# Optimization experiments

Measured on AMD Instinct MI355X. Metric: run time of the kernel, lower is better.

The kernel has to match this reference:

```python
import math
import jax, jax.numpy as jnp
import numpy as np

NEG_INF = -1e9

def setup_inputs() -> dict:
    key = jax.random.key(0)
    k1, k2, k3, k4, k5 = jax.random.split(key, 5)
    B, H, Q, K, D = 4, 16, 1024, 1024, 64
    return {
        "query": jax.random.normal(k1, (B, H, Q, D), dtype=jnp.float32),
        "key": jax.random.normal(k2, (B, H, K, D), dtype=jnp.float32),
        "value": jax.random.normal(k3, (B, H, K, D), dtype=jnp.float32),
        "bigr_k": jax.random.normal(k4, (Q, K, D), dtype=jnp.float32),
        "bigr_v": jax.random.normal(k5, (Q, K, D), dtype=jnp.float32),
    }

def reference(query, key, value, bigr_k, bigr_v):
    # scores: content term + relative-position key term
    scores = jnp.einsum('bhqd,bhkd->bhqk', query, key)
    scores = scores + jnp.einsum('bhqd,qkd->bhqk', query, bigr_k)
    scores = scores / math.sqrt(query.shape[-1])
    # one_direction=True -> causal (lower-triangular) mask
    Qn, Kn = scores.shape[-2], scores.shape[-1]
    causal = jnp.tril(jnp.ones((Qn, Kn), dtype=bool))
    scores = jnp.where(causal, scores, NEG_INF)
    p_attn = jax.nn.softmax(scores, axis=-1)
    output = jnp.einsum('bhqk,bhkd->bhqd', p_attn, value)
    output = output + jnp.einsum('bhqv,qvd->bhqd', p_attn, bigr_v)
    return (output, p_attn)
```

## Files before the change

kernel.cpp:

```cpp
#include <hip/hip_runtime.h>
#include <hip/hip_bf16.h>


#define BH 64
#define SQ 1024
#define SK 1024
#define DH 64
#define SCALE 0.125f

typedef __attribute__((ext_vector_type(4))) float f32x4;
typedef __attribute__((ext_vector_type(8))) unsigned short ushort8;
typedef __attribute__((ext_vector_type(8))) __bf16 bf16x8;

static __device__ inline unsigned short f2bf(float x) {
    unsigned u = __float_as_uint(x);
    unsigned r = u + 0x7FFFu + ((u >> 16) & 1u);
    return (unsigned short)(r >> 16);
}
static __device__ inline float bf2f(unsigned short s) {
    return __uint_as_float(((unsigned)s) << 16);
}

struct Frag2 { bf16x8 h, l; };

static __device__ inline Frag2 load_split(const float* __restrict__ p, float scale) {
    float4 x0 = *reinterpret_cast<const float4*>(p);
    float4 x1 = *reinterpret_cast<const float4*>(p + 4);
    float v[8] = {x0.x, x0.y, x0.z, x0.w, x1.x, x1.y, x1.z, x1.w};
    ushort8 uh, ul;
#pragma unroll
    for (int j = 0; j < 8; ++j) {
        float s = v[j] * scale;
        unsigned short h = f2bf(s);
        float r = s - bf2f(h);
        uh[j] = h;
        ul[j] = f2bf(r);
    }
    Frag2 f;
    f.h = __builtin_bit_cast(bf16x8, uh);
    f.l = __builtin_bit_cast(bf16x8, ul);
    return f;
}

static __device__ inline bf16x8 pack_bf8(float4 x0, float4 x1) {
    float v[8] = {x0.x, x0.y, x0.z, x0.w, x1.x, x1.y, x1.z, x1.w};
    ushort8 u;
#pragma unroll
    for (int j = 0; j < 8; ++j) u[j] = f2bf(v[j]);
    return __builtin_bit_cast(bf16x8, u);
}

static __device__ inline bf16x8 load_bf8(const float* __restrict__ p) {
    float4 x0 = *reinterpret_cast<const float4*>(p);
    float4 x1 = *reinterpret_cast<const float4*>(p + 4);
    return pack_bf8(x0, x1);
}

static __device__ inline bf16x8 load_bf8_strided(const float* __restrict__ p, int stride) {
    ushort8 u;
#pragma unroll
    for (int j = 0; j < 8; ++j) u[j] = f2bf(p[(size_t)j * stride]);
    return __builtin_bit_cast(bf16x8, u);
}

#define MFMA(a, b, c) __builtin_amdgcn_mfma_f32_16x16x32_bf16((a), (b), (c), 0, 0, 0)

#define GLLD(g, s)                                                              \
    __builtin_amdgcn_global_load_lds(                                           \
        (const __attribute__((address_space(1))) void*)(g),                     \
        (__attribute__((address_space(3))) void*)(s), 16, 0, 0)

#define STAGE64(src0, b)                                                        \
    do {                                                                        \
        _Pragma("unroll")                                                       \
        for (int j_ = 0; j_ < 4; ++j_) {                                        \
            const int idx_ = w * 256 + j_ * 64 + l;                             \
            const int row_ = idx_ >> 4;                                         \
            const int g_ = (idx_ & 15) ^ (row_ & 7);                            \
            GLLD((src0) + (size_t)row_ * DH + g_ * 4,                           \
                 &buf[b][w * 256 + j_ * 64]);                                   \
        }                                                                       \
    } while (0)

#define WAITVN(n)                                                               \
    do {                                                                        \
        asm volatile("s_waitcnt vmcnt(" #n ")" ::: "memory");                   \
        __builtin_amdgcn_sched_barrier(0);                                      \
    } while (0)

__global__ __launch_bounds__(256, 4) void k_scores(const float* __restrict__ qp,
                                                   const float* __restrict__ kp,
                                                   float* __restrict__ P) {
    __shared__ float4 buf[2][1024];
    const int bid = blockIdx.x;
    const int qt = bid >> 6;
    const int bh = bid & 63;
    const int tid = threadIdx.x;
    const int w = tid >> 6, l = tid & 63;
    const int lm = l & 15, lg = l >> 4;
    const int q0 = qt * 64;

    Frag2 qh0[4], qh1[4];
#pragma unroll
    for (int nt = 0; nt < 4; ++nt) {
        const float* qrow = qp + ((size_t)bh * SQ + q0 + nt * 16 + lm) * DH + lg * 8;
        qh0[nt] = load_split(qrow, SCALE);
        qh1[nt] = load_split(qrow + 32, SCALE);
    }
    const float* kb = kp + (size_t)bh * SK * DH;
    const int nt_ = qt + 1;

    STAGE64(kb, 0);
#pragma unroll 1
    for (int t = 0; t < nt_; ++t) {
        if (t + 1 < nt_) {
            STAGE64(kb + (size_t)(t + 1) * 64 * DH, (t + 1) & 1);
            WAITVN(4);
        } else {
            WAITVN(0);
        }
        const float4* L = buf[t & 1];
        const int R = w * 16 + lm;
        const int sw = R & 7;
        float4 f0 = L[R * 16 + ((2 * lg) ^ sw)];
        float4 f1 = L[R * 16 + ((2 * lg + 1) ^ sw)];
        float4 f2 = L[R * 16 + ((8 + 2 * lg) ^ sw)];
        float4 f3 = L[R * 16 + ((9 + 2 * lg) ^ sw)];
        bf16x8 alo = pack_bf8(f0, f1);
        bf16x8 ahi = pack_bf8(f2, f3);
        const int kq = t * 64 + w * 16 + lg * 4;
        const bool diag = (t == qt);
#pragma unroll
        for (int nt = 0; nt < 4; ++nt) {
            f32x4 acc = {0.f, 0.f, 0.f, 0.f};
            acc = MFMA(alo, qh0[nt].h, acc);
            acc = MFMA(alo, qh0[nt].l, acc);
            acc = MFMA(ahi, qh1[nt].h, acc);
            acc = MFMA(ahi, qh1[nt].l, acc);
            const int qe = q0 + nt * 16 + lm;
            float ov[4];
#pragma unroll
            for (int r = 0; r < 4; ++r)
                ov[r] = (!diag || (kq + r <= qe)) ? acc[r] : 0.f;
            float4 o;
            o.x = ov[0]; o.y = ov[1]; o.z = ov[2]; o.w = ov[3];
            *reinterpret_cast<float4*>(&P[((size_t)bh * SQ + qe) * SK + kq]) = o;
        }
    }
    const float4 z = {0.f, 0.f, 0.f, 0.f};
#pragma unroll 1
    for (int t = nt_; t < 16; ++t) {
        const int kq = t * 64 + w * 16 + lg * 4;
#pragma unroll
        for (int nt = 0; nt < 4; ++nt) {
            const int qe = q0 + nt * 16 + lm;
            *reinterpret_cast<float4*>(&P[((size_t)bh * SQ + qe) * SK + kq]) = z;
        }
    }
}

__global__ __launch_bounds__(256) void k_rel_pv(const float* __restrict__ query,
                                                const float* __restrict__ bigr_k,
                                                const float* __restrict__ bigr_v,
                                                float* __restrict__ P,
                                                float* __restrict__ out,
                                                float* __restrict__ rs) {
    __shared__ float4 buf[2][1024];
    __shared__ float red[4][64];
    __shared__ float rsum[64];
    int q;
    {
        const int bid = blockIdx.x, c = bid & 255;
        switch (bid >> 8) {
            case 0:  q = 1023 - c; break;
            case 1:  q = c;        break;
            case 2:  q = 767 - c;  break;
            default: q = 256 + c;  break;
        }
    }
    const int KE = q + 1;
    const int nt_ = (KE + 63) >> 6;
    const int tid = threadIdx.x;
    const int w = tid >> 6, l = tid & 63;
    const int lm = l & 15, lg = l >> 4;

    Frag2 qh0[4], qh1[4];
    float* prow[4];
#pragma unroll
    for (int nt = 0; nt < 4; ++nt) {
        const int bh = nt * 16 + lm;
        const float* qrow = query + ((size_t)bh * SQ + q) * DH + lg * 8;
        qh0[nt] = load_split(qrow, SCALE);
        qh1[nt] = load_split(qrow + 32, SCALE);
        prow[nt] = P + ((size_t)bh * SQ + q) * SK;
    }
    const float* bk = bigr_k + (size_t)q * SK * DH;
    const float* bv = bigr_v + (size_t)q * SK * DH;
    float lsum[4] = {0.f, 0.f, 0.f, 0.f};
    f32x4 pr[4][4];
#pragma unroll
    for (int a = 0; a < 4; ++a)
#pragma unroll
        for (int b = 0; b < 4; ++b) pr[a][b] = (f32x4){0.f, 0.f, 0.f, 0.f};

    STAGE64(bk, 0);
#pragma unroll 1
    for (int t = 0; t < nt_; ++t) {
        const int kq = t * 64 + w * 16 + lg * 4;
        float4 pc[4];
#pragma unroll
        for (int nt = 0; nt < 4; ++nt)
            pc[nt] = *reinterpret_cast<const float4*>(prow[nt] + kq);
        bf16x8 bvf[4];
        {
            const int kbw = t * 64 + w * 16 + 4 * lg;
#pragma unroll
            for (int ntd = 0; ntd < 4; ++ntd) {
                ushort8 u;
#pragma unroll
                for (int j = 0; j < 4; ++j)
                    u[j] = f2bf(bv[(size_t)(kbw + j) * DH + ntd * 16 + lm]);
                u[4] = 0; u[5] = 0; u[6] = 0; u[7] = 0;
                bvf[ntd] = __builtin_bit_cast(bf16x8, u);
            }
        }
        if (t + 1 < nt_) {
            STAGE64(bk + (size_t)(t + 1) * 64 * DH, (t + 1) & 1);
            WAITVN(4);
        } else {
            WAITVN(0);
        }
        const float4* L = buf[t & 1];
        const int R = w * 16 + lm;
        const int sw = R & 7;
        float4 f0 = L[R * 16 + ((2 * lg) ^ sw)];
        float4 f1 = L[R * 16 + ((2 * lg + 1) ^ sw)];
        float4 f2 = L[R * 16 + ((8 + 2 * lg) ^ sw)];
        float4 f3 = L[R * 16 + ((9 + 2 * lg) ^ sw)];
        bf16x8 alo = pack_bf8(f0, f1);
        bf16x8 ahi = pack_bf8(f2, f3);
#pragma unroll
        for (int nt = 0; nt < 4; ++nt) {
            f32x4 acc = {0.f, 0.f, 0.f, 0.f};
            acc = MFMA(alo, qh0[nt].h, acc);
            acc = MFMA(alo, qh0[nt].l, acc);
            acc = MFMA(ahi, qh1[nt].h, acc);
            acc = MFMA(ahi, qh1[nt].l, acc);
            const float4 c = pc[nt];
            float cv[4] = {c.x, c.y, c.z, c.w};
            float ov[4];
#pragma unroll
            for (int r = 0; r < 4; ++r) {
                float e = (kq + r < KE) ? __expf(cv[r] + acc[r]) : 0.f;
                ov[r] = e;
                lsum[nt] += e;
            }
            float4 o;
            o.x = ov[0]; o.y = ov[1]; o.z = ov[2]; o.w = ov[3];
            *reinterpret_cast<float4*>(prow[nt] + kq) = o;
            ushort8 ua;
#pragma unroll
            for (int j = 0; j < 4; ++j) ua[j] = f2bf(ov[j]);
            ua[4] = 0; ua[5] = 0; ua[6] = 0; ua[7] = 0;
            bf16x8 af = __builtin_bit_cast(bf16x8, ua);
#pragma unroll
            for (int ntd = 0; ntd < 4; ++ntd)
                pr[nt][ntd] = MFMA(af, bvf[ntd], pr[nt][ntd]);
        }
    }

#pragma unroll
    for (int nt = 0; nt < 4; ++nt) {
        float v = lsum[nt];
        v += __shfl_xor(v, 16);
        v += __shfl_xor(v, 32);
        if (l < 16) red[w][nt * 16 + l] = v;
    }
    __syncthreads();
    if (tid < 64) {
        float nr = 1.0f / (red[0][tid] + red[1][tid] + red[2][tid] + red[3][tid]);
        rsum[tid] = nr;
        rs[(size_t)q * 64 + tid] = nr;
    }
    float* prbuf = reinterpret_cast<float*>(&buf[0][0]);
    if (w < 2) {
        float* dst = prbuf + w * 4096;
#pragma unroll
        for (int nt = 0; nt < 4; ++nt)
#pragma unroll
            for (int ntd = 0; ntd < 4; ++ntd)
#pragma unroll
                for (int r = 0; r < 4; ++r)
                    dst[(nt * 16 + lg * 4 + r) * 64 + ntd * 16 + lm] = pr[nt][ntd][r];
    }
    __syncthreads();
    if (w >= 2) {
        float* dst = prbuf + (w - 2) * 4096;
#pragma unroll
        for (int nt = 0; nt < 4; ++nt)
#pragma unroll
            for (int ntd = 0; ntd < 4; ++ntd)
#pragma unroll
                for (int r = 0; r < 4; ++r)
                    dst[(nt * 16 + lg * 4 + r) * 64 + ntd * 16 + lm] += pr[nt][ntd][r];
    }
    __syncthreads();
#pragma unroll
    for (int i = 0; i < 4; ++i) {
        const int f4i = tid + i * 256;
        float4 a = reinterpret_cast<const float4*>(prbuf)[f4i];
        float4 b = reinterpret_cast<const float4*>(prbuf)[1024 + f4i];
        const int fl = f4i * 4;
        const int bh = fl >> 6, d = fl & 63;
        const float nr = rsum[bh];
        float4 o = {(a.x + b.x) * nr, (a.y + b.y) * nr,
                    (a.z + b.z) * nr, (a.w + b.w) * nr};
        *reinterpret_cast<float4*>(&out[((size_t)bh * SQ + q) * DH + d]) = o;
    }
}

__global__ __launch_bounds__(256) void k_pv(float* __restrict__ P,
                                            const float* __restrict__ V,
                                            const float* __restrict__ rs,
                                            float* __restrict__ out) {
    const int bid = blockIdx.x;
    const int qt = bid >> 6;
    const int bh = bid & 63;
    const int tid = threadIdx.x;
    const int w = tid >> 6, l = tid & 63;
    const int lm = l & 15, lg = l >> 4;
    const int q0 = qt * 64 + w * 16;

    const float wrecip = rs[(size_t)(q0 + lm) * 64 + bh];
    float orecip[4];
#pragma unroll
    for (int r = 0; r < 4; ++r)
        orecip[r] = rs[(size_t)(q0 + lg * 4 + r) * 64 + bh];

    f32x4 acc[4] = {{0.f,0.f,0.f,0.f},{0.f,0.f,0.f,0.f},{0.f,0.f,0.f,0.f},{0.f,0.f,0.f,0.f}};
    const int kend = q0 + 16;
    for (int k0 = 0; k0 < kend; k0 += 32) {
        float* arow = P + ((size_t)bh * SQ + q0 + lm) * SK + k0 + lg * 8;
        float4 x0 = *reinterpret_cast<const float4*>(arow);
        float4 x1 = *reinterpret_cast<const float4*>(arow + 4);
        float4 y0 = {x0.x * wrecip, x0.y * wrecip, x0.z * wrecip, x0.w * wrecip};
        float4 y1 = {x1.x * wrecip, x1.y * wrecip, x1.z * wrecip, x1.w * wrecip};
        *reinterpret_cast<float4*>(arow) = y0;
        *reinterpret_cast<float4*>(arow + 4) = y1;
        bf16x8 a = pack_bf8(x0, x1);
#pragma unroll
        for (int nt = 0; nt < 4; ++nt) {
            const float* bcol = V + ((size_t)bh * SK + k0 + lg * 8) * DH + nt * 16 + lm;
            bf16x8 b = load_bf8_strided(bcol, DH);
            acc[nt] = MFMA(a, b, acc[nt]);
        }
    }
#pragma unroll
    for (int nt = 0; nt < 4; ++nt)
#pragma unroll
        for (int r = 0; r < 4; ++r)
            out[((size_t)bh * SQ + q0 + lg * 4 + r) * DH + nt * 16 + lm] +=
                acc[nt][r] * orecip[r];
}

extern "C" void kernel_launch(void* const* d_in, const int* in_sizes, int n_in,
                              void* d_out, int out_size, void* d_ws, size_t ws_size,
                              hipStream_t stream) {
    const float* query  = (const float*)d_in[0];
    const float* key    = (const float*)d_in[1];
    const float* value  = (const float*)d_in[2];
    const float* bigr_k = (const float*)d_in[3];
    const float* bigr_v = (const float*)d_in[4];
    float* out = (float*)d_out;
    float* P   = out + (size_t)BH * SQ * DH;
    float* rs  = (float*)d_ws;

    k_scores<<<dim3(1024), 256, 0, stream>>>(query, key, P);
    k_rel_pv<<<dim3(SQ), 256, 0, stream>>>(query, bigr_k, bigr_v, P, out, rs);
    k_pv<<<dim3(1024), 256, 0, stream>>>(P, value, rs, out);
}
```

Before: 405.0 us.

## Split relative-position kernel over key range into two blocks per query

The k_rel_pv grid gains a second dimension that splits each query row's key tiles into two halves, so each block handles about half the bigr_k/bigr_v stream. Partial row sums are written per half and combined in k_pv, which now computes the reciprocal and applies normalization after adding the content PV term. Partial output contributions are accumulated with float atomics into an output buffer zeroed by an added memset. This trades more blocks and shorter per-block serial chains for atomic traffic, an extra memset and duplicated per-block setup of query fragments.

```diff
diff --git a/kernel.cpp b/kernel.cpp
--- a/kernel.cpp
+++ b/kernel.cpp
@@ -164,10 +164,9 @@
                                                 const float* __restrict__ bigr_v,
                                                 float* __restrict__ P,
                                                 float* __restrict__ out,
-                                                float* __restrict__ rs) {
+                                                float* __restrict__ ls) {
     __shared__ float4 buf[2][1024];
     __shared__ float red[4][64];
-    __shared__ float rsum[64];
     int q;
     {
         const int bid = blockIdx.x, c = bid & 255;
@@ -178,11 +177,19 @@
             default: q = 256 + c;  break;
         }
     }
+    const int h = blockIdx.y;
     const int KE = q + 1;
     const int nt_ = (KE + 63) >> 6;
+    const int tA = h ? ((nt_ + 1) >> 1) : 0;
+    const int tB = h ? nt_ : ((nt_ + 1) >> 1);
     const int tid = threadIdx.x;
     const int w = tid >> 6, l = tid & 63;
     const int lm = l & 15, lg = l >> 4;
+    float* lsq = ls + ((size_t)q * 2 + h) * 64;
+    if (tA >= tB) {
+        if (tid < 64) lsq[tid] = 0.f;
+        return;
+    }
 
     Frag2 qh0[4], qh1[4];
     float* prow[4];
@@ -203,9 +210,9 @@
 #pragma unroll
         for (int b = 0; b < 4; ++b) pr[a][b] = (f32x4){0.f, 0.f, 0.f, 0.f};
 
-    STAGE64(bk, 0);
+    STAGE64(bk + (size_t)tA * 64 * DH, tA & 1);
 #pragma unroll 1
-    for (int t = 0; t < nt_; ++t) {
+    for (int t = tA; t < tB; ++t) {
         const int kq = t * 64 + w * 16 + lg * 4;
         float4 pc[4];
 #pragma unroll
@@ -224,7 +231,7 @@
                 bvf[ntd] = __builtin_bit_cast(bf16x8, u);
             }
         }
-        if (t + 1 < nt_) {
+        if (t + 1 < tB) {
             STAGE64(bk + (size_t)(t + 1) * 64 * DH, (t + 1) & 1);
             WAITVN(4);
         } else {
@@ -277,11 +284,8 @@
         if (l < 16) red[w][nt * 16 + l] = v;
     }
     __syncthreads();
-    if (tid < 64) {
-        float nr = 1.0f / (red[0][tid] + red[1][tid] + red[2][tid] + red[3][tid]);
-        rsum[tid] = nr;
-        rs[(size_t)q * 64 + tid] = nr;
-    }
+    if (tid < 64)
+        lsq[tid] = red[0][tid] + red[1][tid] + red[2][tid] + red[3][tid];
     float* prbuf = reinterpret_cast<float*>(&buf[0][0]);
     if (w < 2) {
         float* dst = prbuf + w * 4096;
@@ -312,16 +316,17 @@
         float4 b = reinterpret_cast<const float4*>(prbuf)[1024 + f4i];
         const int fl = f4i * 4;
         const int bh = fl >> 6, d = fl & 63;
-        const float nr = rsum[bh];
-        float4 o = {(a.x + b.x) * nr, (a.y + b.y) * nr,
-                    (a.z + b.z) * nr, (a.w + b.w) * nr};
-        *reinterpret_cast<float4*>(&out[((size_t)bh * SQ + q) * DH + d]) = o;
+        float* dst = &out[((size_t)bh * SQ + q) * DH + d];
+        atomicAdd(dst + 0, a.x + b.x);
+        atomicAdd(dst + 1, a.y + b.y);
+        atomicAdd(dst + 2, a.z + b.z);
+        atomicAdd(dst + 3, a.w + b.w);
     }
 }
 
 __global__ __launch_bounds__(256) void k_pv(float* __restrict__ P,
                                             const float* __restrict__ V,
-                                            const float* __restrict__ rs,
+                                            const float* __restrict__ ls,
                                             float* __restrict__ out) {
     const int bid = blockIdx.x;
     const int qt = bid >> 6;
@@ -331,11 +336,14 @@
     const int lm = l & 15, lg = l >> 4;
     const int q0 = qt * 64 + w * 16;
 
-    const float wrecip = rs[(size_t)(q0 + lm) * 64 + bh];
+    const float wrecip =
+        1.0f / (ls[(size_t)(q0 + lm) * 128 + bh] +
+                ls[(size_t)(q0 + lm) * 128 + 64 + bh]);
     float orecip[4];
 #pragma unroll
     for (int r = 0; r < 4; ++r)
-        orecip[r] = rs[(size_t)(q0 + lg * 4 + r) * 64 + bh];
+        orecip[r] = 1.0f / (ls[(size_t)(q0 + lg * 4 + r) * 128 + bh] +
+                            ls[(size_t)(q0 + lg * 4 + r) * 128 + 64 + bh]);
 
     f32x4 acc[4] = {{0.f,0.f,0.f,0.f},{0.f,0.f,0.f,0.f},{0.f,0.f,0.f,0.f},{0.f,0.f,0.f,0.f}};
     const int kend = q0 + 16;
@@ -358,9 +366,10 @@
 #pragma unroll
     for (int nt = 0; nt < 4; ++nt)
 #pragma unroll
-        for (int r = 0; r < 4; ++r)
-            out[((size_t)bh * SQ + q0 + lg * 4 + r) * DH + nt * 16 + lm] +=
-                acc[nt][r] * orecip[r];
+        for (int r = 0; r < 4; ++r) {
+            float* op = &out[((size_t)bh * SQ + q0 + lg * 4 + r) * DH + nt * 16 + lm];
+            *op = (*op + acc[nt][r]) * orecip[r];
+        }
 }
 
 extern "C" void kernel_launch(void* const* d_in, const int* in_sizes, int n_in,
@@ -373,9 +382,10 @@
     const float* bigr_v = (const float*)d_in[4];
     float* out = (float*)d_out;
     float* P   = out + (size_t)BH * SQ * DH;
-    float* rs  = (float*)d_ws;
-
+    float* ls  = (float*)d_ws;
+
+    hipMemsetAsync(out, 0, (size_t)BH * SQ * DH * sizeof(float), stream);
     k_scores<<<dim3(1024), 256, 0, stream>>>(query, key, P);
-    k_rel_pv<<<dim3(SQ), 256, 0, stream>>>(query, bigr_k, bigr_v, P, out, rs);
-    k_pv<<<dim3(1024), 256, 0, stream>>>(P, value, rs, out);
-}
+    k_rel_pv<<<dim3(1024, 2), 256, 0, stream>>>(query, bigr_k, bigr_v, P, out, ls);
+    k_pv<<<dim3(1024), 256, 0, stream>>>(P, value, ls, out);
+}
```

Result: slower. 432.6 us (+6.8%).

## Deepen prefetch pipeline to two stages for bigr_k tiles and P/bigr_v loads

Applied to the files above, without the earlier changes.

Restructures the main loop into an even/odd unrolled pipeline. The next iteration's P row and bigr_v values are loaded into registers while the current tile is computed, and bigr_k is staged into LDS two tiles ahead instead of one. The goal is to hide global memory latency behind the MFMA and exp work. In exchange it uses more registers, which can lower occupancy, and it depends on vmcnt wait counts being exactly right.

```diff
diff --git a/kernel.cpp b/kernel.cpp
--- a/kernel.cpp
+++ b/kernel.cpp
@@ -203,33 +203,23 @@
 #pragma unroll
         for (int b = 0; b < 4; ++b) pr[a][b] = (f32x4){0.f, 0.f, 0.f, 0.f};
 
-    STAGE64(bk, 0);
-#pragma unroll 1
-    for (int t = 0; t < nt_; ++t) {
+    float4 pcE[4], pcO[4];
+    float bvE[16], bvO[16];
+
+    auto loadPC = [&](float4 (&pc)[4], float (&bvr)[16], int t) {
         const int kq = t * 64 + w * 16 + lg * 4;
-        float4 pc[4];
 #pragma unroll
         for (int nt = 0; nt < 4; ++nt)
             pc[nt] = *reinterpret_cast<const float4*>(prow[nt] + kq);
-        bf16x8 bvf[4];
-        {
-            const int kbw = t * 64 + w * 16 + 4 * lg;
-#pragma unroll
-            for (int ntd = 0; ntd < 4; ++ntd) {
-                ushort8 u;
-#pragma unroll
-                for (int j = 0; j < 4; ++j)
-                    u[j] = f2bf(bv[(size_t)(kbw + j) * DH + ntd * 16 + lm]);
-                u[4] = 0; u[5] = 0; u[6] = 0; u[7] = 0;
-                bvf[ntd] = __builtin_bit_cast(bf16x8, u);
-            }
-        }
-        if (t + 1 < nt_) {
-            STAGE64(bk + (size_t)(t + 1) * 64 * DH, (t + 1) & 1);
-            WAITVN(4);
-        } else {
-            WAITVN(0);
-        }
+        const int kbw = t * 64 + w * 16 + 4 * lg;
+#pragma unroll
+        for (int ntd = 0; ntd < 4; ++ntd)
+#pragma unroll
+            for (int j = 0; j < 4; ++j)
+                bvr[ntd * 4 + j] = bv[(size_t)(kbw + j) * DH + ntd * 16 + lm];
+    };
+
+    auto compute = [&](int t, const float4 (&pc)[4], const float (&bvr)[16]) {
         const float4* L = buf[t & 1];
         const int R = w * 16 + lm;
         const int sw = R & 7;
@@ -239,6 +229,17 @@
         float4 f3 = L[R * 16 + ((9 + 2 * lg) ^ sw)];
         bf16x8 alo = pack_bf8(f0, f1);
         bf16x8 ahi = pack_bf8(f2, f3);
+        if (t + 2 < nt_) STAGE64(bk + (size_t)(t + 2) * 64 * DH, t & 1);
+        bf16x8 bvf[4];
+#pragma unroll
+        for (int ntd = 0; ntd < 4; ++ntd) {
+            ushort8 u;
+#pragma unroll
+            for (int j = 0; j < 4; ++j) u[j] = f2bf(bvr[ntd * 4 + j]);
+            u[4] = 0; u[5] = 0; u[6] = 0; u[7] = 0;
+            bvf[ntd] = __builtin_bit_cast(bf16x8, u);
+        }
+        const int kq = t * 64 + w * 16 + lg * 4;
 #pragma unroll
         for (int nt = 0; nt < 4; ++nt) {
             f32x4 acc = {0.f, 0.f, 0.f, 0.f};
@@ -266,6 +267,29 @@
 #pragma unroll
             for (int ntd = 0; ntd < 4; ++ntd)
                 pr[nt][ntd] = MFMA(af, bvf[ntd], pr[nt][ntd]);
+        }
+    };
+
+    STAGE64(bk, 0);
+    loadPC(pcE, bvE, 0);
+    if (nt_ > 1) STAGE64(bk + (size_t)64 * DH, 1);
+#pragma unroll 1
+    for (int t = 0; t < nt_; t += 2) {
+        if (t + 1 < nt_) {
+            loadPC(pcO, bvO, t + 1);
+            WAITVN(28);
+        } else {
+            WAITVN(4);
+        }
+        compute(t, pcE, bvE);
+        if (t + 1 < nt_) {
+            if (t + 2 < nt_) {
+                loadPC(pcE, bvE, t + 2);
+                WAITVN(28);
+            } else {
+                WAITVN(4);
+            }
+            compute(t + 1, pcO, bvO);
         }
     }
 
```

Result: slower. 421.2 us (+4.0%).
